# Kernel optimization log

Hardware: AMD Instinct MI355X
Metric: run time of the kernel (lower is better)

The kernel has to match this reference:

```python
import jax, jax.numpy as jnp
import numpy as np

D_MODEL, D_STATE, EXPAND = 1024, 16, 2
D_INNER = EXPAND * D_MODEL
BATCH, SEQ = 4, 4096


def setup_inputs() -> dict:
    key = jax.random.key(0)
    ks = jax.random.split(key, 9)
    s = 0.02
    return {
        "x": jax.random.normal(ks[0], (BATCH, SEQ, D_MODEL), jnp.float32),
        # torch Linear weight [out,in] stored transposed here as [in,out]
        "W_in": jax.random.normal(ks[1], (D_MODEL, 2 * D_INNER), jnp.float32) * s,
        "conv_w": jax.random.normal(ks[2], (D_INNER, 1, 3), jnp.float32) * s,  # depthwise, groups=D_INNER
        "conv_b": jax.random.normal(ks[3], (D_INNER,), jnp.float32) * s,
        "W_B": jax.random.normal(ks[4], (D_INNER, D_STATE), jnp.float32) * s,
        "W_C": jax.random.normal(ks[5], (D_INNER, D_STATE), jnp.float32) * s,
        "A": jax.random.normal(ks[6], (D_STATE,), jnp.float32),
        "D": jnp.ones((D_INNER,), jnp.float32),
        "W_out": jax.random.normal(ks[7], (D_INNER, D_MODEL), jnp.float32) * s,
    }


def reference(x, W_in, conv_w, conv_b, W_B, W_C, A, D, W_out):
    d_inner = conv_w.shape[0]
    # input projection and split into main / residual gate paths
    xr = jnp.einsum("bld,de->ble", x, W_in)  # [B, L, 2*d_inner]
    x_main, res = xr[..., :d_inner], xr[..., d_inner:]
    # depthwise conv1d along seq (kernel 3, pad 1)
    xc = jax.lax.conv_general_dilated(
        x_main.transpose(0, 2, 1), conv_w, (1,), [(1, 1)],
        dimension_numbers=("NCH", "OIH", "NCH"), feature_group_count=d_inner)
    xc = (xc + conv_b[None, :, None]).transpose(0, 2, 1)  # [B, L, d_inner]
    xc = jax.nn.silu(xc)
    # selective-scan inputs
    Bt = jnp.einsum("bli,is->bls", xc, W_B)  # [B, L, d_state]
    Ct = jnp.einsum("bli,is->bls", xc, W_C)
    decay = jnp.exp(-jax.nn.softplus(A))  # exp(A_diag), [d_state]

    def step(state, bc):
        b_t, c_t = bc
        state = state * decay + b_t  # i=0: zeros*decay + B[0] == B[0]
        return state, jnp.sum(state * c_t, axis=-1)  # scalar per batch

    _, ys = jax.lax.scan(step, jnp.zeros_like(Bt[:, 0]),
                         (Bt.transpose(1, 0, 2), Ct.transpose(1, 0, 2)))
    ys = ys.T  # [B, L]
    y = ys[..., None] + xc * D  # broadcast scan output across d_inner
    y = y * jax.nn.silu(res)
    return jnp.einsum("bli,id->bld", y, W_out)
```

## Files before the change

kernel.cpp:

```cpp
#include <hip/hip_runtime.h>


typedef _Float16 half8 __attribute__((ext_vector_type(8)));
typedef float floatx4 __attribute__((ext_vector_type(4)));

#define D_MODEL 1024
#define D_INNER 2048
#define SEQ     4096
#define NBATCH  4
#define NROWS   (NBATCH * SEQ)

__device__ __forceinline__ void async16(_Float16* lds, const _Float16* g) {
    __builtin_amdgcn_global_load_lds((const __attribute__((address_space(1))) void*)g,
                                     (__attribute__((address_space(3))) void*)lds, 16, 0, 0);
}

__device__ __forceinline__ float siluf(float x) {
    return x / (1.f + __expf(-x));
}


__global__ __launch_bounds__(256) void convert_f32_f16(const float* __restrict__ src,
                                                       _Float16* __restrict__ dst) {
    size_t idx = ((size_t)blockIdx.x * 256 + threadIdx.x) * 8;
    float4 a = *(const float4*)(src + idx);
    float4 b = *(const float4*)(src + idx + 4);
    half8 o = {(_Float16)a.x, (_Float16)a.y, (_Float16)a.z, (_Float16)a.w,
               (_Float16)b.x, (_Float16)b.y, (_Float16)b.z, (_Float16)b.w};
    *(half8*)(dst + idx) = o;
}

__global__ __launch_bounds__(256) void transpose_to_f16(const float* __restrict__ src,
                                                        _Float16* __restrict__ dst,
                                                        int K, int N) {
    __shared__ float tile[32][33];
    int n0 = blockIdx.x * 32, k0 = blockIdx.y * 32;
    int x = threadIdx.x, y = threadIdx.y;
#pragma unroll
    for (int r = 0; r < 32; r += 8)
        tile[y + r][x] = src[(size_t)(k0 + y + r) * N + (n0 + x)];
    __syncthreads();
#pragma unroll
    for (int r = 0; r < 32; r += 8)
        dst[(size_t)(n0 + y + r) * K + (k0 + x)] = (_Float16)tile[x][y + r];
}

__global__ __launch_bounds__(256) void convert_wbct(const float* __restrict__ WB,
                                                    const float* __restrict__ WC,
                                                    _Float16* __restrict__ WBCT) {
    int idx = blockIdx.x * 256 + threadIdx.x;
    int n = idx >> 11, k = idx & 2047;
    float v = (n < 16) ? WB[k * 16 + n] : WC[k * 16 + (n - 16)];
    WBCT[idx] = (_Float16)v;
}

template <typename OutT>
__global__ __launch_bounds__(256) void gemm_tn(const _Float16* __restrict__ A,
                                               const _Float16* __restrict__ BT,
                                               OutT* __restrict__ C,
                                               int M, int N, int K) {
    __shared__ __align__(16) _Float16 As[128 * 64];
    __shared__ __align__(16) _Float16 Bs[128 * 64];
    const int tid = threadIdx.x;
    const int wid = tid >> 6, lane = tid & 63;
    const int row0 = blockIdx.y * 128, col0 = blockIdx.x * 128;
    const int wm = (wid & 1) * 64, wn = (wid >> 1) * 64;

    floatx4 acc[4][4] = {};

    const int sr = lane >> 3;
    const int sc = ((lane & 7) ^ sr) * 8;
    const size_t aBase = (size_t)(row0 + wid * 32 + sr) * K + sc;
    const size_t bBase = (size_t)(col0 + wid * 32 + sr) * K + sc;
    _Float16* ldsA = As + wid * 2048;
    _Float16* ldsB = Bs + wid * 2048;

    const int fr = lane & 15, q = lane >> 4;
    const int frq = fr & 7;

    for (int k0 = 0; k0 < K; k0 += 64) {
        __syncthreads();
#pragma unroll
        for (int t = 0; t < 4; t++) {
            async16(ldsA + t * 512, A + aBase + (size_t)(t * 8) * K + k0);
            async16(ldsB + t * 512, BT + bBase + (size_t)(t * 8) * K + k0);
        }
        __syncthreads();
#pragma unroll
        for (int kk = 0; kk < 2; kk++) {
            const int sw = (((kk << 2) + q) ^ frq) * 8;
            half8 af[4], bf[4];
#pragma unroll
            for (int i = 0; i < 4; i++) {
                af[i] = *(const half8*)(As + (wm + i * 16 + fr) * 64 + sw);
                bf[i] = *(const half8*)(Bs + (wn + i * 16 + fr) * 64 + sw);
            }
#pragma unroll
            for (int i = 0; i < 4; i++)
#pragma unroll
                for (int j = 0; j < 4; j++)
                    acc[i][j] = __builtin_amdgcn_mfma_f32_16x16x32_f16(af[i], bf[j], acc[i][j], 0, 0, 0);
        }
    }

    const int er = (lane >> 4) * 4, ec = lane & 15;
#pragma unroll
    for (int i = 0; i < 4; i++)
#pragma unroll
        for (int j = 0; j < 4; j++)
#pragma unroll
            for (int r = 0; r < 4; r++) {
                int row = row0 + wm + i * 16 + er + r;
                int col = col0 + wn + j * 16 + ec;
                C[(size_t)row * N + col] = (OutT)acc[i][j][r];
            }
}

__global__ __launch_bounds__(256) void bc_gemm(const _Float16* __restrict__ A,
                                               const _Float16* __restrict__ BT,
                                               float* __restrict__ C) {
    const int K = D_INNER;
    __shared__ __align__(16) _Float16 As[64 * 64];
    __shared__ __align__(16) _Float16 Bs[32 * 64];
    const int tid = threadIdx.x, wid = tid >> 6, lane = tid & 63;
    const int row0 = blockIdx.x * 64;
    floatx4 acc[2] = {};

    const int srow = lane >> 3;
    const int scol = (lane & 7) * 8;
    const size_t aOff0 = (size_t)(row0 + wid * 16 + srow) * K + scol;
    const size_t aOff1 = aOff0 + (size_t)8 * K;
    const size_t bOff  = (size_t)(wid * 8 + srow) * K + scol;
    _Float16* ldsA = As + wid * 1024;
    _Float16* ldsB = Bs + wid * 512;
    const int fr = lane & 15, fc = (lane >> 4) * 8;

    for (int k0 = 0; k0 < K; k0 += 64) {
        __syncthreads();
        async16(ldsA,       A + aOff0 + k0);
        async16(ldsA + 512, A + aOff1 + k0);
        async16(ldsB,       BT + bOff + k0);
        __syncthreads();
#pragma unroll
        for (int s = 0; s < 2; s++) {
            half8 af = *(const half8*)(As + (wid * 16 + fr) * 64 + s * 32 + fc);
#pragma unroll
            for (int nj = 0; nj < 2; nj++) {
                half8 bf = *(const half8*)(Bs + (nj * 16 + fr) * 64 + s * 32 + fc);
                acc[nj] = __builtin_amdgcn_mfma_f32_16x16x32_f16(af, bf, acc[nj], 0, 0, 0);
            }
        }
    }
    const int er = (lane >> 4) * 4, ec = lane & 15;
#pragma unroll
    for (int nj = 0; nj < 2; nj++)
#pragma unroll
        for (int r = 0; r < 4; r++)
            C[(size_t)(row0 + wid * 16 + er + r) * 32 + nj * 16 + ec] = acc[nj][r];
}

__global__ __launch_bounds__(256) void conv_silu(const _Float16* __restrict__ xr,
                                                 const float* __restrict__ cw,
                                                 const float* __restrict__ cb,
                                                 _Float16* __restrict__ xc) {
    int row = blockIdx.x;
    int l = row & (SEQ - 1);
    int i = threadIdx.x * 8;
    const _Float16* cur = xr + (size_t)row * 4096 + i;
    half8 c8 = *(const half8*)cur;
    half8 p8 = {}, n8 = {};
    if (l > 0)       p8 = *(const half8*)(cur - 4096);
    if (l < SEQ - 1) n8 = *(const half8*)(cur + 4096);
    half8 o;
#pragma unroll
    for (int j = 0; j < 8; j++) {
        int ii = i + j;
        float a = (float)p8[j] * cw[ii * 3] + (float)c8[j] * cw[ii * 3 + 1] +
                  (float)n8[j] * cw[ii * 3 + 2] + cb[ii];
        o[j] = (_Float16)siluf(a);
    }
    *(half8*)(xc + (size_t)row * D_INNER + i) = o;
}

__global__ __launch_bounds__(1024) void scan_kernel(const float* __restrict__ BtCt,
                                                    const float* __restrict__ A,
                                                    float* __restrict__ ys) {
    const int b = blockIdx.x, t = threadIdx.x;
    const int c = t >> 4, s = t & 15;
    const float decay = __expf(-log1pf(__expf(A[s])));
    const size_t base = (size_t)b * SEQ * 32;
    const int l0 = c * 64;

    float st = 0.f;
    for (int j = 0; j < 64; j++)
        st = st * decay + BtCt[base + (size_t)(l0 + j) * 32 + s];

    __shared__ float fin[64][16];
    __shared__ float carry[64][16];
    fin[c][s] = st;
    __syncthreads();
    if (t < 16) {
        float d64 = decay;
#pragma unroll
        for (int k = 0; k < 6; k++) d64 *= d64;
        float cy = 0.f;
        for (int cc = 0; cc < 64; cc++) {
            carry[cc][s] = cy;
            cy = cy * d64 + fin[cc][s];
        }
    }
    __syncthreads();

    st = carry[c][s];
    for (int j = 0; j < 64; j++) {
        size_t r = base + (size_t)(l0 + j) * 32;
        st = st * decay + BtCt[r + s];
        float y = st * BtCt[r + 16 + s];
        y += __shfl_xor(y, 1, 16);
        y += __shfl_xor(y, 2, 16);
        y += __shfl_xor(y, 4, 16);
        y += __shfl_xor(y, 8, 16);
        if (s == 0) ys[b * SEQ + l0 + j] = y;
    }
}

__global__ __launch_bounds__(256) void fuse_y(const float* __restrict__ ys,
                                              const float* __restrict__ D,
                                              const _Float16* __restrict__ xr,
                                              _Float16* __restrict__ xc) {
    int row = blockIdx.x;
    int i = threadIdx.x * 8;
    float yv = ys[row];
    half8 x8 = *(const half8*)(xc + (size_t)row * D_INNER + i);
    half8 r8 = *(const half8*)(xr + (size_t)row * 4096 + 2048 + i);
    half8 o;
#pragma unroll
    for (int j = 0; j < 8; j++) {
        float y = yv + (float)x8[j] * D[i + j];
        o[j] = (_Float16)(y * siluf((float)r8[j]));
    }
    *(half8*)(xc + (size_t)row * D_INNER + i) = o;
}

extern "C" void kernel_launch(void* const* d_in, const int* in_sizes, int n_in,
                              void* d_out, int out_size, void* d_ws, size_t ws_size,
                              hipStream_t stream) {
    const float* x      = (const float*)d_in[0];
    const float* W_in   = (const float*)d_in[1];
    const float* conv_w = (const float*)d_in[2];
    const float* conv_b = (const float*)d_in[3];
    const float* W_B    = (const float*)d_in[4];
    const float* W_C    = (const float*)d_in[5];
    const float* A      = (const float*)d_in[6];
    const float* D      = (const float*)d_in[7];
    const float* W_out  = (const float*)d_in[8];
    float* out = (float*)d_out;

    char* ws = (char*)d_ws;
    size_t off = 0;
    auto alloc = [&](size_t bytes) { size_t o = off; off += (bytes + 255) & ~(size_t)255; return o; };
    _Float16* xh    = (_Float16*)(ws + alloc((size_t)NROWS * D_MODEL * 2));
    _Float16* WinT  = (_Float16*)(ws + alloc((size_t)4096 * 1024 * 2));
    _Float16* WoutT = (_Float16*)(ws + alloc((size_t)1024 * 2048 * 2));
    _Float16* WBCT  = (_Float16*)(ws + alloc((size_t)32 * 2048 * 2));
    _Float16* xr    = (_Float16*)(ws + alloc((size_t)NROWS * 4096 * 2));
    _Float16* xc    = (_Float16*)(ws + alloc((size_t)NROWS * D_INNER * 2));
    float*    BtCt  = (float*)(ws + alloc((size_t)NROWS * 32 * 4));
    float*    ysbuf = (float*)(ws + alloc((size_t)NROWS * 4));

    convert_f32_f16<<<(NROWS * D_MODEL) / (256 * 8), 256, 0, stream>>>(x, xh);
    transpose_to_f16<<<dim3(4096 / 32, 1024 / 32), dim3(32, 8), 0, stream>>>(W_in, WinT, 1024, 4096);
    transpose_to_f16<<<dim3(1024 / 32, 2048 / 32), dim3(32, 8), 0, stream>>>(W_out, WoutT, 2048, 1024);
    convert_wbct<<<(32 * 2048) / 256, 256, 0, stream>>>(W_B, W_C, WBCT);
    gemm_tn<_Float16><<<dim3(4096 / 128, NROWS / 128), 256, 0, stream>>>(xh, WinT, xr, NROWS, 4096, 1024);
    conv_silu<<<NROWS, 256, 0, stream>>>(xr, conv_w, conv_b, xc);
    bc_gemm<<<NROWS / 64, 256, 0, stream>>>(xc, WBCT, BtCt);
    scan_kernel<<<NBATCH, 1024, 0, stream>>>(BtCt, A, ysbuf);
    fuse_y<<<NROWS, 256, 0, stream>>>(ysbuf, D, xr, xc);
    gemm_tn<float><<<dim3(1024 / 128, NROWS / 128), 256, 0, stream>>>(xc, WoutT, out, NROWS, 1024, 2048);
}
```

Baseline: 530.7 us.

## Split scan into three-phase chunked scan and fuse output pass into final phase

Replaces the single 4-block scan kernel with a three-phase chunked scan. Phase one computes per-chunk final states across many blocks, phase two runs the cross-chunk carry serially, and phase three redoes the intra-chunk scan and fuses in the y/gating elementwise pass. The aim is to use the whole GPU instead of 4 workgroups during the scan and to drop the separate fuse_y launch and the ys round trip. The cost is an extra launch and a serial 256-step carry loop in a single 64-thread block.

```diff
diff --git a/kernel.cpp b/kernel.cpp
--- a/kernel.cpp
+++ b/kernel.cpp
@@ -9,6 +9,9 @@
 #define SEQ     4096
 #define NBATCH  4
 #define NROWS   (NBATCH * SEQ)
+#define CHUNK   16
+#define NCHUNK  (SEQ / CHUNK)
+#define NTASK   (NBATCH * NCHUNK)
 
 __device__ __forceinline__ void async16(_Float16* lds, const _Float16* g) {
     __builtin_amdgcn_global_load_lds((const __attribute__((address_space(1))) void*)g,
@@ -17,6 +20,10 @@
 
 __device__ __forceinline__ float siluf(float x) {
     return x / (1.f + __expf(-x));
+}
+
+__device__ __forceinline__ float decay_of(const float* A, int s) {
+    return __expf(-log1pf(__expf(A[s])));
 }
 
 
@@ -182,64 +189,90 @@
     *(half8*)(xc + (size_t)row * D_INNER + i) = o;
 }
 
-__global__ __launch_bounds__(1024) void scan_kernel(const float* __restrict__ BtCt,
+
+__global__ __launch_bounds__(256) void scan_p1(const float* __restrict__ BtCt,
+                                               const float* __restrict__ A,
+                                               float* __restrict__ fin) {
+    int g = blockIdx.x * 256 + threadIdx.x;
+    int task = g >> 4, s = g & 15;
+    int b = task >> 8, c = task & (NCHUNK - 1);
+    const float decay = decay_of(A, s);
+    size_t r = ((size_t)b * SEQ + c * CHUNK) * 32;
+    float st = 0.f;
+#pragma unroll
+    for (int j = 0; j < CHUNK; j++)
+        st = st * decay + BtCt[r + (size_t)j * 32 + s];
+    fin[task * 16 + s] = st;
+}
+
+__global__ __launch_bounds__(64) void scan_p2(const float* __restrict__ fin,
+                                              const float* __restrict__ A,
+                                              float* __restrict__ carry) {
+    int t = threadIdx.x;
+    int b = t >> 4, s = t & 15;
+    float decay = decay_of(A, s);
+    float d16 = decay;
+#pragma unroll
+    for (int k = 0; k < 4; k++) d16 *= d16;
+    float cy = 0.f;
+    for (int c = 0; c < NCHUNK; c++) {
+        int idx = ((b * NCHUNK) + c) * 16 + s;
+        carry[idx] = cy;
+        cy = cy * d16 + fin[idx];
+    }
+}
+
+__global__ __launch_bounds__(256) void scan_p3_fuse(const float* __restrict__ BtCt,
                                                     const float* __restrict__ A,
-                                                    float* __restrict__ ys) {
-    const int b = blockIdx.x, t = threadIdx.x;
-    const int c = t >> 4, s = t & 15;
-    const float decay = __expf(-log1pf(__expf(A[s])));
-    const size_t base = (size_t)b * SEQ * 32;
-    const int l0 = c * 64;
-
-    float st = 0.f;
-    for (int j = 0; j < 64; j++)
-        st = st * decay + BtCt[base + (size_t)(l0 + j) * 32 + s];
-
-    __shared__ float fin[64][16];
-    __shared__ float carry[64][16];
-    fin[c][s] = st;
+                                                    const float* __restrict__ carry,
+                                                    const float* __restrict__ D,
+                                                    const _Float16* __restrict__ xr,
+                                                    _Float16* __restrict__ xc) {
+    __shared__ float ysl[CHUNK];
+    const int task = blockIdx.x;
+    const int b = task >> 8, c = task & (NCHUNK - 1);
+    const int row0 = b * SEQ + c * CHUNK;
+    const int tid = threadIdx.x;
+
+    if (tid < 16) {
+        const int s = tid;
+        const float decay = decay_of(A, s);
+        float st = carry[task * 16 + s];
+        size_t r = (size_t)row0 * 32;
+#pragma unroll
+        for (int j = 0; j < CHUNK; j++) {
+            st = st * decay + BtCt[r + s];
+            float y = st * BtCt[r + 16 + s];
+            y += __shfl_xor(y, 1, 16);
+            y += __shfl_xor(y, 2, 16);
+            y += __shfl_xor(y, 4, 16);
+            y += __shfl_xor(y, 8, 16);
+            if (s == 0) ysl[j] = y;
+            r += 32;
+        }
+    }
     __syncthreads();
-    if (t < 16) {
-        float d64 = decay;
-#pragma unroll
-        for (int k = 0; k < 6; k++) d64 *= d64;
-        float cy = 0.f;
-        for (int cc = 0; cc < 64; cc++) {
-            carry[cc][s] = cy;
-            cy = cy * d64 + fin[cc][s];
-        }
-    }
-    __syncthreads();
-
-    st = carry[c][s];
-    for (int j = 0; j < 64; j++) {
-        size_t r = base + (size_t)(l0 + j) * 32;
-        st = st * decay + BtCt[r + s];
-        float y = st * BtCt[r + 16 + s];
-        y += __shfl_xor(y, 1, 16);
-        y += __shfl_xor(y, 2, 16);
-        y += __shfl_xor(y, 4, 16);
-        y += __shfl_xor(y, 8, 16);
-        if (s == 0) ys[b * SEQ + l0 + j] = y;
-    }
-}
-
-__global__ __launch_bounds__(256) void fuse_y(const float* __restrict__ ys,
-                                              const float* __restrict__ D,
-                                              const _Float16* __restrict__ xr,
-                                              _Float16* __restrict__ xc) {
-    int row = blockIdx.x;
-    int i = threadIdx.x * 8;
-    float yv = ys[row];
-    half8 x8 = *(const half8*)(xc + (size_t)row * D_INNER + i);
-    half8 r8 = *(const half8*)(xr + (size_t)row * 4096 + 2048 + i);
-    half8 o;
-#pragma unroll
-    for (int j = 0; j < 8; j++) {
-        float y = yv + (float)x8[j] * D[i + j];
-        o[j] = (_Float16)(y * siluf((float)r8[j]));
-    }
-    *(half8*)(xc + (size_t)row * D_INNER + i) = o;
+
+#pragma unroll
+    for (int it = 0; it < 16; it++) {
+        int chunk = it * 256 + tid;
+        int rl = chunk >> 8;
+        int colb = (chunk & 255) * 8;
+        size_t row = (size_t)(row0 + rl);
+        float yv = ysl[rl];
+        half8 x8 = *(const half8*)(xc + row * D_INNER + colb);
+        half8 r8 = *(const half8*)(xr + row * 4096 + 2048 + colb);
+        float4 d0 = *(const float4*)(D + colb);
+        float4 d1 = *(const float4*)(D + colb + 4);
+        half8 o;
+        float dd[8] = {d0.x, d0.y, d0.z, d0.w, d1.x, d1.y, d1.z, d1.w};
+#pragma unroll
+        for (int j = 0; j < 8; j++) {
+            float y = yv + (float)x8[j] * dd[j];
+            o[j] = (_Float16)(y * siluf((float)r8[j]));
+        }
+        *(half8*)(xc + row * D_INNER + colb) = o;
+    }
 }
 
 extern "C" void kernel_launch(void* const* d_in, const int* in_sizes, int n_in,
@@ -266,7 +299,8 @@
     _Float16* xr    = (_Float16*)(ws + alloc((size_t)NROWS * 4096 * 2));
     _Float16* xc    = (_Float16*)(ws + alloc((size_t)NROWS * D_INNER * 2));
     float*    BtCt  = (float*)(ws + alloc((size_t)NROWS * 32 * 4));
-    float*    ysbuf = (float*)(ws + alloc((size_t)NROWS * 4));
+    float*    fin   = (float*)(ws + alloc((size_t)NTASK * 16 * 4));
+    float*    carry = (float*)(ws + alloc((size_t)NTASK * 16 * 4));
 
     convert_f32_f16<<<(NROWS * D_MODEL) / (256 * 8), 256, 0, stream>>>(x, xh);
     transpose_to_f16<<<dim3(4096 / 32, 1024 / 32), dim3(32, 8), 0, stream>>>(W_in, WinT, 1024, 4096);
@@ -275,7 +309,8 @@
     gemm_tn<_Float16><<<dim3(4096 / 128, NROWS / 128), 256, 0, stream>>>(xh, WinT, xr, NROWS, 4096, 1024);
     conv_silu<<<NROWS, 256, 0, stream>>>(xr, conv_w, conv_b, xc);
     bc_gemm<<<NROWS / 64, 256, 0, stream>>>(xc, WBCT, BtCt);
-    scan_kernel<<<NBATCH, 1024, 0, stream>>>(BtCt, A, ysbuf);
-    fuse_y<<<NROWS, 256, 0, stream>>>(ysbuf, D, xr, xc);
+    scan_p1<<<NTASK * 16 / 256, 256, 0, stream>>>(BtCt, A, fin);
+    scan_p2<<<1, 64, 0, stream>>>(fin, A, carry);
+    scan_p3_fuse<<<NTASK, 256, 0, stream>>>(BtCt, A, carry, D, xr, xc);
     gemm_tn<float><<<dim3(1024 / 128, NROWS / 128), 256, 0, stream>>>(xc, WoutT, out, NROWS, 1024, 2048);
 }
```

Result: faster. 518.3 us (-2.3%).
